# Kernel optimization log

Measured on AMD Instinct MI355X. Metric: run time of the kernel, lower is better.

The kernel has to match this reference:

```python
import jax, jax.numpy as jnp
import numpy as np

ALPHA = 3.0


def _conv3x3(x, W, b):
    # x: [N, C, H, W]; W: [O, I, 3, 3]; SAME padding, stride 1 (matches Conv2d(dim, dim, 3, 1, 1))
    y = jax.lax.conv_general_dilated(
        x, W, window_strides=(1, 1), padding='SAME',
        dimension_numbers=('NCHW', 'OIHW', 'NCHW'))
    return y + b[None, :, None, None]


def setup_inputs() -> dict:
    key = jax.random.key(0)
    k = jax.random.split(key, 5)
    b, m, z, x, y = 2, 5, 64, 128, 256
    fan_in = z * 3 * 3
    bound = 1.0 / np.sqrt(fan_in)
    pts = jax.random.normal(k[0], (b, m, z, x, y), dtype=jnp.float32)
    W1 = jax.random.uniform(k[1], (z, z, 3, 3), jnp.float32, -bound, bound)
    b1 = jax.random.uniform(k[2], (z,), jnp.float32, -bound, bound)
    W2 = jax.random.uniform(k[3], (z, z, 3, 3), jnp.float32, -bound, bound)
    b2 = jax.random.uniform(k[4], (z,), jnp.float32, -bound, bound)
    return {"pts": pts, "W1": W1, "b1": b1, "W2": W2, "b2": b2}


def reference(pts, W1, b1, W2, b2):
    b, m, z, x, y = pts.shape
    flat = pts.reshape(b * m, z, x, y)
    n1 = jnp.tanh(ALPHA * _conv3x3(flat, W1, b1)).reshape(b, m, z, x, y)
    n2 = jnp.tanh(ALPHA * _conv3x3(flat, W2, b2)).reshape(b, m, z, x, y)
    # s[b,m,n,x,y] = sum_l n1[b,m,l,x,y] * n2[b,n,l,x,y]; second einsum is s with m,n swapped
    s = jnp.einsum('bmlxy,bnlxy->bmnxy', n1, n2)
    a = s - jnp.swapaxes(s, 1, 2)
    adj = jax.nn.sigmoid(ALPHA * a)
    adj = adj + jnp.eye(m, dtype=adj.dtype)[None, :, :, None, None]
    adj = adj / jnp.sum(adj, axis=2, keepdims=True)
    return adj
```

## Files before the change

### kernel.cpp

```cpp
#include <hip/hip_runtime.h>
#include <hip/hip_bf16.h>

typedef _Float16 f16x8 __attribute__((ext_vector_type(8)));
typedef float f32x4 __attribute__((ext_vector_type(4)));

constexpr int B_ = 2, M_ = 5, C_ = 64, H_ = 128, W_ = 256;
constexpr int HW_ = H_ * W_;
constexpr int PLANE_ = C_ * HW_;
constexpr int NIMG_ = B_ * M_;
constexpr int PH_ = H_ + 2, PW_ = W_ + 2;

constexpr size_t OFF_XIN = 256;
constexpr size_t SZ_XIN  = (size_t)NIMG_ * PH_ * PW_ * 64 * 2;
constexpr size_t OFF_WL1 = OFF_XIN + SZ_XIN;
constexpr size_t SZ_WL   = (size_t)9 * 64 * 64 * 2;
constexpr size_t OFF_WL2 = OFF_WL1 + SZ_WL;
constexpr size_t OFF_N1  = OFF_WL2 + SZ_WL;
constexpr size_t SZ_N    = (size_t)NIMG_ * HW_ * 64 * 2;
constexpr size_t OFF_N2  = OFF_N1 + SZ_N;

__global__ void sniff_kernel(const unsigned short* __restrict__ pts,
                             int* __restrict__ flag) {
  int lane = threadIdx.x;
  unsigned short v = pts[2 * lane];
  int e = (v >> 7) & 0xFF;
  unsigned long long mask = __ballot(e >= 100 && e <= 140);
  if (lane == 0) flag[0] = (__popcll(mask) >= 48) ? 1 : 0;
}

__global__ void border_zero(_Float16* __restrict__ x) {
  int idx = blockIdx.x * 256 + threadIdx.x;
  if (idx >= NIMG_ * 772) return;
  int img = idx / 772, r = idx - img * 772;
  int ph, pw;
  if (r < 258)      { ph = 0;            pw = r; }
  else if (r < 516) { ph = PH_ - 1;      pw = r - 258; }
  else if (r < 644) { ph = r - 516 + 1;  pw = 0; }
  else              { ph = r - 644 + 1;  pw = PW_ - 1; }
  f16x8 z = {};
  _Float16* p = x + ((size_t)(img * PH_ + ph) * PW_ + pw) * 64;
#pragma unroll
  for (int c8 = 0; c8 < 8; ++c8) *(f16x8*)(p + c8 * 8) = z;
}

__global__ __launch_bounds__(256) void prep_kernel(const void* __restrict__ in,
                                                   _Float16* __restrict__ xin,
                                                   const int* __restrict__ flag) {
  __shared__ float sT[64 * 65];
  const int t = threadIdx.x;
  const int wt = blockIdx.x, h = blockIdx.y, img = blockIdx.z;
  const bool isb = flag[0] != 0;
  const size_t ibase = (size_t)img * PLANE_ + (size_t)h * W_ + wt * 64;
#pragma unroll
  for (int k = 0; k < 16; ++k) {
    int idx = k * 256 + t;
    int ic = idx >> 6, w = idx & 63;
    size_t g = ibase + (size_t)ic * HW_ + w;
    float v = isb ? __bfloat162float(((const __hip_bfloat16*)in)[g])
                  : ((const float*)in)[g];
    sT[ic * 65 + w] = v;
  }
  __syncthreads();
#pragma unroll
  for (int k = 0; k < 2; ++k) {
    int idx = k * 256 + t;
    int w = idx >> 3, c8 = idx & 7;
    f16x8 vv;
#pragma unroll
    for (int j = 0; j < 8; ++j) vv[j] = (_Float16)sT[(c8 * 8 + j) * 65 + w];
    int pw = wt * 64 + w + 1;
    size_t rowbase = ((size_t)(img * PH_ + (h + 1)) * PW_ + pw) * 128;
    int off = (c8 * 16) ^ ((pw & 7) << 4);
    *(f16x8*)((char*)xin + rowbase + off) = vv;
  }
}

__global__ void wprep_kernel(const void* __restrict__ W1, const void* __restrict__ W2,
                             _Float16* __restrict__ wl1, _Float16* __restrict__ wl2,
                             const int* __restrict__ flag) {
  int idx = blockIdx.x * 256 + threadIdx.x;
  const bool isb = flag[0] != 0;
  const void* Wsrc = blockIdx.y ? W2 : W1;
  _Float16* dst = blockIdx.y ? wl2 : wl1;
  int tap = idx >> 12;
  int oc = (idx >> 6) & 63;
  int ic = idx & 63;
  size_t s = (size_t)(oc * 64 + ic) * 9 + tap;
  float v = isb ? __bfloat162float(((const __hip_bfloat16*)Wsrc)[s])
                : ((const float*)Wsrc)[s];
  dst[(tap * 4096 + oc * 64 + ic) ^ ((oc & 7) << 3)] = (_Float16)v;
}

__global__ __launch_bounds__(512, 2)
void conv_fused(const _Float16* __restrict__ xin,
                const _Float16* __restrict__ wl1, const _Float16* __restrict__ wl2,
                const void* __restrict__ bias1, const void* __restrict__ bias2,
                const int* __restrict__ flag,
                _Float16* __restrict__ n1, _Float16* __restrict__ n2) {
  __shared__ _Float16 sIn[10 * 66 * 64];
  __shared__ _Float16 sW[2 * 9 * 32 * 64];

  const int t = threadIdx.x;
  const int och = blockIdx.x & 1;
  const int pid = blockIdx.x >> 1;

  const int l = t & 63, wv = t >> 6;
  const int lr = l & 15, hi = l >> 4;
  const bool isb = flag[0] != 0;

#pragma unroll
  for (int c = 0; c < 2; ++c) {
    const f16x8* src = (const f16x8*)((const char*)(c ? wl2 : wl1) + och * 4096);
    f16x8* dst = (f16x8*)sW + c * 2304;
    for (int i = t; i < 2304; i += 512) {
      int tap = i >> 8, e = i & 255;
      dst[i] = src[tap * 512 + e];
    }
  }

  float bv1[2], bv2[2];
#pragma unroll
  for (int ob = 0; ob < 2; ++ob) {
    int oc = och * 32 + ob * 16 + lr;
    bv1[ob] = isb ? __bfloat162float(((const __hip_bfloat16*)bias1)[oc])
                  : ((const float*)bias1)[oc];
    bv2[ob] = isb ? __bfloat162float(((const __hip_bfloat16*)bias2)[oc])
                  : ((const float*)bias2)[oc];
  }

  int c2a[3][2], c2b[2];
#pragma unroll
  for (int dx = 0; dx < 3; ++dx) {
    int key = (((l & 7) + dx) & 7) << 4;
#pragma unroll
    for (int kw = 0; kw < 2; ++kw) c2a[dx][kw] = (hi * 16 + kw * 64) ^ key;
  }
#pragma unroll
  for (int kw = 0; kw < 2; ++kw) c2b[kw] = (hi * 16 + kw * 64) ^ ((l & 7) << 4);

  f16x8 rg[11];
  auto issue = [&](int tt) {
    int img = tt >> 6, hy = (tt >> 2) & 15, wx = tt & 3;
    const f16x8* base = (const f16x8*)(xin + ((size_t)(img * PH_ + hy * 8) * PW_ + wx * 64) * 64);
#pragma unroll
    for (int u = 0; u < 11; ++u) {
      int i = u * 512 + t;
      if (u < 10 || i < 5280) {
        int r = i / 528, cc = i - r * 528;
        rg[u] = base[(size_t)r * (PW_ * 8) + cc];
      }
    }
  };

  issue(pid);

  const char* sInB = (const char*)sIn;
  const char* sWB = (const char*)sW;

#pragma unroll 1
  for (int j = 0; j < 5; ++j) {
    const int tt = pid + 128 * j;

#pragma unroll
    for (int u = 0; u < 11; ++u) {
      int i = u * 512 + t;
      if (u < 10 || i < 5280) ((f16x8*)sIn)[i] = rg[u];
    }
    __syncthreads();

    if (j < 4) issue(pid + 128 * (j + 1));

    f32x4 acc1[4][2], acc2[4][2];
#pragma unroll
    for (int pa = 0; pa < 4; ++pa)
#pragma unroll
      for (int ob = 0; ob < 2; ++ob) {
        acc1[pa][ob] = (f32x4){0.f, 0.f, 0.f, 0.f};
        acc2[pa][ob] = (f32x4){0.f, 0.f, 0.f, 0.f};
      }

#pragma unroll
    for (int ky = 0; ky < 3; ++ky) {
#pragma unroll
      for (int kx = 0; kx < 3; ++kx) {
        const int tap = ky * 3 + kx;
#pragma unroll
        for (int kw = 0; kw < 2; ++kw) {
          f16x8 a[4], b1[2], b2[2];
#pragma unroll
          for (int pa = 0; pa < 4; ++pa)
            a[pa] = *(const f16x8*)(sInB + ((wv + ky) * 8448 + (pa * 16 + lr + kx) * 128 + c2a[kx][kw]));
#pragma unroll
          for (int ob = 0; ob < 2; ++ob) {
            b1[ob] = *(const f16x8*)(sWB + (tap * 4096 + (ob * 16 + lr) * 128 + c2b[kw]));
            b2[ob] = *(const f16x8*)(sWB + (36864 + tap * 4096 + (ob * 16 + lr) * 128 + c2b[kw]));
          }
#pragma unroll
          for (int pa = 0; pa < 4; ++pa)
#pragma unroll
            for (int ob = 0; ob < 2; ++ob) {
              acc1[pa][ob] = __builtin_amdgcn_mfma_f32_16x16x32_f16(a[pa], b1[ob], acc1[pa][ob], 0, 0, 0);
              acc2[pa][ob] = __builtin_amdgcn_mfma_f32_16x16x32_f16(a[pa], b2[ob], acc2[pa][ob], 0, 0, 0);
            }
        }
      }
    }

    {
      int img = tt >> 6, hy = (tt >> 2) & 15, wx = tt & 3;
      size_t rowbase = ((size_t)(img * H_ + hy * 8 + wv) * W_ + wx * 64) * 64 + och * 32 + lr;
#pragma unroll
      for (int pa = 0; pa < 4; ++pa)
#pragma unroll
        for (int ob = 0; ob < 2; ++ob)
#pragma unroll
          for (int r = 0; r < 4; ++r) {
            int px = pa * 16 + hi * 4 + r;
            size_t o = rowbase + (size_t)px * 64 + ob * 16;
            float u1 = acc1[pa][ob][r] + bv1[ob];
            u1 = fminf(fmaxf(u1, -8.f), 8.f);
            float e1 = __builtin_exp2f(u1 * -8.656170245f);
            n1[o] = (_Float16)((1.f - e1) * __builtin_amdgcn_rcpf(1.f + e1));
            float u2 = acc2[pa][ob][r] + bv2[ob];
            u2 = fminf(fmaxf(u2, -8.f), 8.f);
            float e2 = __builtin_exp2f(u2 * -8.656170245f);
            n2[o] = (_Float16)((1.f - e2) * __builtin_amdgcn_rcpf(1.f + e2));
          }
    }
    __syncthreads();
  }
}

__global__ __launch_bounds__(256)
void pairwise_kernel(const _Float16* __restrict__ n1, const _Float16* __restrict__ n2,
                     void* __restrict__ out, const int* __restrict__ flag) {
  int tid = blockIdx.x * 256 + threadIdx.x;
  int gp = tid >> 3;
  int j = tid & 7;
  int b = gp >> 15, px = gp & (HW_ - 1);
  const _Float16* p1 = n1 + ((size_t)(b * M_) * HW_ + px) * 64 + j * 8;
  const _Float16* p2 = n2 + ((size_t)(b * M_) * HW_ + px) * 64 + j * 8;

  f16x8 A[M_], Bv[M_];
#pragma unroll
  for (int m = 0; m < M_; ++m) {
    A[m]  = *(const f16x8*)(p1 + (size_t)m * PLANE_);
    Bv[m] = *(const f16x8*)(p2 + (size_t)m * PLANE_);
  }

  float s[M_][M_];
#pragma unroll
  for (int m = 0; m < M_; ++m)
#pragma unroll
    for (int n = 0; n < M_; ++n) s[m][n] = 0.f;

#pragma unroll
  for (int jj = 0; jj < 8; ++jj)
#pragma unroll
    for (int m = 0; m < M_; ++m)
#pragma unroll
      for (int n = 0; n < M_; ++n)
        s[m][n] += (float)A[m][jj] * (float)Bv[n][jj];

#pragma unroll
  for (int m = 0; m < M_; ++m)
#pragma unroll
    for (int n = 0; n < M_; ++n) {
      s[m][n] += __shfl_xor(s[m][n], 1);
      s[m][n] += __shfl_xor(s[m][n], 2);
      s[m][n] += __shfl_xor(s[m][n], 4);
    }

  float adj[M_][M_], rs[M_];
#pragma unroll
  for (int m = 0; m < M_; ++m) {
    float r = 0.f;
#pragma unroll
    for (int n = 0; n < M_; ++n) {
      float a = s[m][n] - s[n][m];
      float e = __builtin_exp2f(a * -4.328085123f);
      float v = __builtin_amdgcn_rcpf(1.f + e);
      if (m == n) v += 1.f;
      adj[m][n] = v;
      r += v;
    }
    rs[m] = r;
  }

  const bool isb = flag[0] != 0;
  for (int k = j; k < 25; k += 8) {
    int m = k / 5, n = k - m * 5;
    float v = adj[m][n] * __builtin_amdgcn_rcpf(rs[m]);
    size_t o = ((size_t)((b * M_ + m) * M_ + n)) * HW_ + px;
    if (isb) ((__hip_bfloat16*)out)[o] = __float2bfloat16(v);
    else     ((float*)out)[o] = v;
  }
}

extern "C" void kernel_launch(void* const* d_in, const int* in_sizes, int n_in,
                              void* d_out, int out_size, void* d_ws, size_t ws_size,
                              hipStream_t stream) {
  const void* pts = d_in[0];
  const void* W1  = d_in[1];
  const void* b1  = d_in[2];
  const void* W2  = d_in[3];
  const void* b2  = d_in[4];

  char* ws = (char*)d_ws;
  int* flag = (int*)ws;
  _Float16* xin = (_Float16*)(ws + OFF_XIN);
  _Float16* wl1 = (_Float16*)(ws + OFF_WL1);
  _Float16* wl2 = (_Float16*)(ws + OFF_WL2);
  _Float16* n1  = (_Float16*)(ws + OFF_N1);
  _Float16* n2  = (_Float16*)(ws + OFF_N2);

  sniff_kernel<<<dim3(1), dim3(64), 0, stream>>>((const unsigned short*)pts, flag);
  border_zero<<<dim3((NIMG_ * 772 + 255) / 256), dim3(256), 0, stream>>>(xin);
  prep_kernel<<<dim3(4, H_, NIMG_), dim3(256), 0, stream>>>(pts, xin, flag);
  wprep_kernel<<<dim3(144, 2), dim3(256), 0, stream>>>(W1, W2, wl1, wl2, flag);
  conv_fused<<<dim3(256), dim3(512), 0, stream>>>(xin, wl1, wl2, b1, b2, flag, n1, n2);
  pairwise_kernel<<<dim3(B_ * HW_ * 8 / 256), dim3(256), 0, stream>>>(n1, n2, d_out, flag);
}
```

Baseline: 134.7 us.

## Split conv output channels across twice as many waves per block

Doubles the conv block to 1024 threads, giving each wave one row and one 16-channel half of the output instead of both halves. This halves per-wave accumulators and register staging, which aims to raise occupancy and latency hiding. Bias is folded into the accumulator init, and the tanh epilogue is simplified to one exp and one fma-based reciprocal form without clamping. The trade-off is more waves re-reading the same input fragments from LDS, and the unclamped exp could overflow for large inputs, though the rcp form tolerates infinity.

```diff
diff --git a/kernel.cpp b/kernel.cpp
--- a/kernel.cpp
+++ b/kernel.cpp
@@ -91,7 +91,7 @@
   dst[(tap * 4096 + oc * 64 + ic) ^ ((oc & 7) << 3)] = (_Float16)v;
 }
 
-__global__ __launch_bounds__(512, 2)
+__global__ __launch_bounds__(1024, 4)
 void conv_fused(const _Float16* __restrict__ xin,
                 const _Float16* __restrict__ wl1, const _Float16* __restrict__ wl2,
                 const void* __restrict__ bias1, const void* __restrict__ bias2,
@@ -104,7 +104,10 @@
   const int och = blockIdx.x & 1;
   const int pid = blockIdx.x >> 1;
 
-  const int l = t & 63, wv = t >> 6;
+  const int l = t & 63;
+  const int w = t >> 6;
+  const int row = w >> 1;
+  const int obh = w & 1;
   const int lr = l & 15, hi = l >> 4;
   const bool isb = flag[0] != 0;
 
@@ -112,21 +115,17 @@
   for (int c = 0; c < 2; ++c) {
     const f16x8* src = (const f16x8*)((const char*)(c ? wl2 : wl1) + och * 4096);
     f16x8* dst = (f16x8*)sW + c * 2304;
-    for (int i = t; i < 2304; i += 512) {
+    for (int i = t; i < 2304; i += 1024) {
       int tap = i >> 8, e = i & 255;
       dst[i] = src[tap * 512 + e];
     }
   }
 
-  float bv1[2], bv2[2];
-#pragma unroll
-  for (int ob = 0; ob < 2; ++ob) {
-    int oc = och * 32 + ob * 16 + lr;
-    bv1[ob] = isb ? __bfloat162float(((const __hip_bfloat16*)bias1)[oc])
-                  : ((const float*)bias1)[oc];
-    bv2[ob] = isb ? __bfloat162float(((const __hip_bfloat16*)bias2)[oc])
-                  : ((const float*)bias2)[oc];
-  }
+  const int myoc = och * 32 + obh * 16 + lr;
+  float bv1 = isb ? __bfloat162float(((const __hip_bfloat16*)bias1)[myoc])
+                  : ((const float*)bias1)[myoc];
+  float bv2 = isb ? __bfloat162float(((const __hip_bfloat16*)bias2)[myoc])
+                  : ((const float*)bias2)[myoc];
 
   int c2a[3][2], c2b[2];
 #pragma unroll
@@ -138,14 +137,14 @@
 #pragma unroll
   for (int kw = 0; kw < 2; ++kw) c2b[kw] = (hi * 16 + kw * 64) ^ ((l & 7) << 4);
 
-  f16x8 rg[11];
+  f16x8 rg[6];
   auto issue = [&](int tt) {
     int img = tt >> 6, hy = (tt >> 2) & 15, wx = tt & 3;
     const f16x8* base = (const f16x8*)(xin + ((size_t)(img * PH_ + hy * 8) * PW_ + wx * 64) * 64);
 #pragma unroll
-    for (int u = 0; u < 11; ++u) {
-      int i = u * 512 + t;
-      if (u < 10 || i < 5280) {
+    for (int u = 0; u < 6; ++u) {
+      int i = u * 1024 + t;
+      if (u < 5 || i < 5280) {
         int r = i / 528, cc = i - r * 528;
         rg[u] = base[(size_t)r * (PW_ * 8) + cc];
       }
@@ -156,28 +155,28 @@
 
   const char* sInB = (const char*)sIn;
   const char* sWB = (const char*)sW;
+  const int boff1 = (obh * 16 + lr) * 128;
+  const int boff2 = 36864 + boff1;
 
 #pragma unroll 1
   for (int j = 0; j < 5; ++j) {
     const int tt = pid + 128 * j;
 
 #pragma unroll
-    for (int u = 0; u < 11; ++u) {
-      int i = u * 512 + t;
-      if (u < 10 || i < 5280) ((f16x8*)sIn)[i] = rg[u];
+    for (int u = 0; u < 6; ++u) {
+      int i = u * 1024 + t;
+      if (u < 5 || i < 5280) ((f16x8*)sIn)[i] = rg[u];
     }
     __syncthreads();
 
     if (j < 4) issue(pid + 128 * (j + 1));
 
-    f32x4 acc1[4][2], acc2[4][2];
-#pragma unroll
-    for (int pa = 0; pa < 4; ++pa)
-#pragma unroll
-      for (int ob = 0; ob < 2; ++ob) {
-        acc1[pa][ob] = (f32x4){0.f, 0.f, 0.f, 0.f};
-        acc2[pa][ob] = (f32x4){0.f, 0.f, 0.f, 0.f};
-      }
+    f32x4 acc1[4], acc2[4];
+#pragma unroll
+    for (int pa = 0; pa < 4; ++pa) {
+      acc1[pa] = (f32x4){bv1, bv1, bv1, bv1};
+      acc2[pa] = (f32x4){bv2, bv2, bv2, bv2};
+    }
 
 #pragma unroll
     for (int ky = 0; ky < 3; ++ky) {
@@ -186,46 +185,35 @@
         const int tap = ky * 3 + kx;
 #pragma unroll
         for (int kw = 0; kw < 2; ++kw) {
-          f16x8 a[4], b1[2], b2[2];
+          f16x8 a[4], b1, b2;
 #pragma unroll
           for (int pa = 0; pa < 4; ++pa)
-            a[pa] = *(const f16x8*)(sInB + ((wv + ky) * 8448 + (pa * 16 + lr + kx) * 128 + c2a[kx][kw]));
-#pragma unroll
-          for (int ob = 0; ob < 2; ++ob) {
-            b1[ob] = *(const f16x8*)(sWB + (tap * 4096 + (ob * 16 + lr) * 128 + c2b[kw]));
-            b2[ob] = *(const f16x8*)(sWB + (36864 + tap * 4096 + (ob * 16 + lr) * 128 + c2b[kw]));
+            a[pa] = *(const f16x8*)(sInB + ((row + ky) * 8448 + (pa * 16 + lr + kx) * 128 + c2a[kx][kw]));
+          b1 = *(const f16x8*)(sWB + tap * 4096 + boff1 + c2b[kw]);
+          b2 = *(const f16x8*)(sWB + tap * 4096 + boff2 + c2b[kw]);
+#pragma unroll
+          for (int pa = 0; pa < 4; ++pa) {
+            acc1[pa] = __builtin_amdgcn_mfma_f32_16x16x32_f16(a[pa], b1, acc1[pa], 0, 0, 0);
+            acc2[pa] = __builtin_amdgcn_mfma_f32_16x16x32_f16(a[pa], b2, acc2[pa], 0, 0, 0);
           }
-#pragma unroll
-          for (int pa = 0; pa < 4; ++pa)
-#pragma unroll
-            for (int ob = 0; ob < 2; ++ob) {
-              acc1[pa][ob] = __builtin_amdgcn_mfma_f32_16x16x32_f16(a[pa], b1[ob], acc1[pa][ob], 0, 0, 0);
-              acc2[pa][ob] = __builtin_amdgcn_mfma_f32_16x16x32_f16(a[pa], b2[ob], acc2[pa][ob], 0, 0, 0);
-            }
         }
       }
     }
 
     {
       int img = tt >> 6, hy = (tt >> 2) & 15, wx = tt & 3;
-      size_t rowbase = ((size_t)(img * H_ + hy * 8 + wv) * W_ + wx * 64) * 64 + och * 32 + lr;
+      size_t rowbase = ((size_t)(img * H_ + hy * 8 + row) * W_ + wx * 64) * 64 + myoc;
 #pragma unroll
       for (int pa = 0; pa < 4; ++pa)
 #pragma unroll
-        for (int ob = 0; ob < 2; ++ob)
-#pragma unroll
-          for (int r = 0; r < 4; ++r) {
-            int px = pa * 16 + hi * 4 + r;
-            size_t o = rowbase + (size_t)px * 64 + ob * 16;
-            float u1 = acc1[pa][ob][r] + bv1[ob];
-            u1 = fminf(fmaxf(u1, -8.f), 8.f);
-            float e1 = __builtin_exp2f(u1 * -8.656170245f);
-            n1[o] = (_Float16)((1.f - e1) * __builtin_amdgcn_rcpf(1.f + e1));
-            float u2 = acc2[pa][ob][r] + bv2[ob];
-            u2 = fminf(fmaxf(u2, -8.f), 8.f);
-            float e2 = __builtin_exp2f(u2 * -8.656170245f);
-            n2[o] = (_Float16)((1.f - e2) * __builtin_amdgcn_rcpf(1.f + e2));
-          }
+        for (int r = 0; r < 4; ++r) {
+          int px = pa * 16 + hi * 4 + r;
+          size_t o = rowbase + (size_t)px * 64;
+          float e1 = __builtin_exp2f(acc1[pa][r] * 8.656170245f);
+          n1[o] = (_Float16)fmaf(-2.f, __builtin_amdgcn_rcpf(1.f + e1), 1.f);
+          float e2 = __builtin_exp2f(acc2[pa][r] * 8.656170245f);
+          n2[o] = (_Float16)fmaf(-2.f, __builtin_amdgcn_rcpf(1.f + e2), 1.f);
+        }
     }
     __syncthreads();
   }
@@ -318,6 +306,6 @@
   border_zero<<<dim3((NIMG_ * 772 + 255) / 256), dim3(256), 0, stream>>>(xin);
   prep_kernel<<<dim3(4, H_, NIMG_), dim3(256), 0, stream>>>(pts, xin, flag);
   wprep_kernel<<<dim3(144, 2), dim3(256), 0, stream>>>(W1, W2, wl1, wl2, flag);
-  conv_fused<<<dim3(256), dim3(512), 0, stream>>>(xin, wl1, wl2, b1, b2, flag, n1, n2);
+  conv_fused<<<dim3(256), dim3(1024), 0, stream>>>(xin, wl1, wl2, b1, b2, flag, n1, n2);
   pairwise_kernel<<<dim3(B_ * HW_ * 8 / 256), dim3(256), 0, stream>>>(n1, n2, d_out, flag);
 }
```

Result: slower. 144.6 us (+7.4%).

## Stage conv input via direct global-to-LDS loads and cache W1 fragments in registers

Applied to the files above, without the earlier changes.

Replaces the register-staged prefetch of the next input tile with direct global_load_lds copies issued right before each tile's compute, followed by a full vmcnt wait. This drops the cross-iteration overlap in exchange for fewer VGPRs. Most of the W1 B-fragments are hoisted into registers for the whole kernel, cutting LDS reads. Bias is folded into the accumulator init, and tanh is rewritten as 1-2/(1+exp(2x)) without clamping. The risks are exposed load latency, higher register pressure from the cached fragments, and possible overflow of exp for large inputs, although rcp of inf yields 0 so the result stays bounded.

```diff
diff --git a/kernel.cpp b/kernel.cpp
--- a/kernel.cpp
+++ b/kernel.cpp
@@ -138,45 +138,52 @@
 #pragma unroll
   for (int kw = 0; kw < 2; ++kw) c2b[kw] = (hi * 16 + kw * 64) ^ ((l & 7) << 4);
 
-  f16x8 rg[11];
-  auto issue = [&](int tt) {
-    int img = tt >> 6, hy = (tt >> 2) & 15, wx = tt & 3;
-    const f16x8* base = (const f16x8*)(xin + ((size_t)(img * PH_ + hy * 8) * PW_ + wx * 64) * 64);
-#pragma unroll
-    for (int u = 0; u < 11; ++u) {
-      int i = u * 512 + t;
-      if (u < 10 || i < 5280) {
-        int r = i / 528, cc = i - r * 528;
-        rg[u] = base[(size_t)r * (PW_ * 8) + cc];
-      }
-    }
-  };
-
-  issue(pid);
-
   const char* sInB = (const char*)sIn;
   const char* sWB = (const char*)sW;
+
+  __syncthreads();
+
+  f16x8 b1r0[9][2];
+  f16x8 b1r1[9];
+#pragma unroll
+  for (int tap = 0; tap < 9; ++tap) {
+#pragma unroll
+    for (int kw = 0; kw < 2; ++kw)
+      b1r0[tap][kw] = *(const f16x8*)(sWB + tap * 4096 + lr * 128 + c2b[kw]);
+    b1r1[tap] = *(const f16x8*)(sWB + tap * 4096 + (16 + lr) * 128 + c2b[0]);
+  }
+
+  auto stage = [&](int tt) {
+    int img = tt >> 6, hy = (tt >> 2) & 15, wx = tt & 3;
+    const _Float16* tb = xin + ((size_t)(img * PH_ + hy * 8) * PW_ + wx * 64) * 64;
+#pragma unroll
+    for (int u = 0; u < 11; ++u) {
+      int c = u * 512 + t;
+      if (u < 10 || c < 5280) {
+        int r = c / 528, cc = c - r * 528;
+        const _Float16* g = tb + (size_t)r * (PW_ * 64) + cc * 8;
+        __builtin_amdgcn_global_load_lds(
+            (const __attribute__((address_space(1))) void*)g,
+            (__attribute__((address_space(3))) void*)(sIn + c * 8), 16, 0, 0);
+      }
+    }
+  };
 
 #pragma unroll 1
   for (int j = 0; j < 5; ++j) {
     const int tt = pid + 128 * j;
 
-#pragma unroll
-    for (int u = 0; u < 11; ++u) {
-      int i = u * 512 + t;
-      if (u < 10 || i < 5280) ((f16x8*)sIn)[i] = rg[u];
-    }
+    stage(tt);
+    asm volatile("s_waitcnt vmcnt(0)" ::: "memory");
     __syncthreads();
 
-    if (j < 4) issue(pid + 128 * (j + 1));
-
     f32x4 acc1[4][2], acc2[4][2];
 #pragma unroll
     for (int pa = 0; pa < 4; ++pa)
 #pragma unroll
       for (int ob = 0; ob < 2; ++ob) {
-        acc1[pa][ob] = (f32x4){0.f, 0.f, 0.f, 0.f};
-        acc2[pa][ob] = (f32x4){0.f, 0.f, 0.f, 0.f};
+        acc1[pa][ob] = (f32x4){bv1[ob], bv1[ob], bv1[ob], bv1[ob]};
+        acc2[pa][ob] = (f32x4){bv2[ob], bv2[ob], bv2[ob], bv2[ob]};
       }
 
 #pragma unroll
@@ -186,22 +193,22 @@
         const int tap = ky * 3 + kx;
 #pragma unroll
         for (int kw = 0; kw < 2; ++kw) {
-          f16x8 a[4], b1[2], b2[2];
+          f16x8 a[4];
 #pragma unroll
           for (int pa = 0; pa < 4; ++pa)
             a[pa] = *(const f16x8*)(sInB + ((wv + ky) * 8448 + (pa * 16 + lr + kx) * 128 + c2a[kx][kw]));
-#pragma unroll
-          for (int ob = 0; ob < 2; ++ob) {
-            b1[ob] = *(const f16x8*)(sWB + (tap * 4096 + (ob * 16 + lr) * 128 + c2b[kw]));
-            b2[ob] = *(const f16x8*)(sWB + (36864 + tap * 4096 + (ob * 16 + lr) * 128 + c2b[kw]));
+          f16x8 b1a = b1r0[tap][kw];
+          f16x8 b1b = (kw == 0) ? b1r1[tap]
+                                : *(const f16x8*)(sWB + tap * 4096 + (16 + lr) * 128 + c2b[1]);
+          f16x8 b2a = *(const f16x8*)(sWB + 36864 + tap * 4096 + lr * 128 + c2b[kw]);
+          f16x8 b2b = *(const f16x8*)(sWB + 36864 + tap * 4096 + (16 + lr) * 128 + c2b[kw]);
+#pragma unroll
+          for (int pa = 0; pa < 4; ++pa) {
+            acc1[pa][0] = __builtin_amdgcn_mfma_f32_16x16x32_f16(a[pa], b1a, acc1[pa][0], 0, 0, 0);
+            acc1[pa][1] = __builtin_amdgcn_mfma_f32_16x16x32_f16(a[pa], b1b, acc1[pa][1], 0, 0, 0);
+            acc2[pa][0] = __builtin_amdgcn_mfma_f32_16x16x32_f16(a[pa], b2a, acc2[pa][0], 0, 0, 0);
+            acc2[pa][1] = __builtin_amdgcn_mfma_f32_16x16x32_f16(a[pa], b2b, acc2[pa][1], 0, 0, 0);
           }
-#pragma unroll
-          for (int pa = 0; pa < 4; ++pa)
-#pragma unroll
-            for (int ob = 0; ob < 2; ++ob) {
-              acc1[pa][ob] = __builtin_amdgcn_mfma_f32_16x16x32_f16(a[pa], b1[ob], acc1[pa][ob], 0, 0, 0);
-              acc2[pa][ob] = __builtin_amdgcn_mfma_f32_16x16x32_f16(a[pa], b2[ob], acc2[pa][ob], 0, 0, 0);
-            }
         }
       }
     }
@@ -217,14 +224,10 @@
           for (int r = 0; r < 4; ++r) {
             int px = pa * 16 + hi * 4 + r;
             size_t o = rowbase + (size_t)px * 64 + ob * 16;
-            float u1 = acc1[pa][ob][r] + bv1[ob];
-            u1 = fminf(fmaxf(u1, -8.f), 8.f);
-            float e1 = __builtin_exp2f(u1 * -8.656170245f);
-            n1[o] = (_Float16)((1.f - e1) * __builtin_amdgcn_rcpf(1.f + e1));
-            float u2 = acc2[pa][ob][r] + bv2[ob];
-            u2 = fminf(fmaxf(u2, -8.f), 8.f);
-            float e2 = __builtin_exp2f(u2 * -8.656170245f);
-            n2[o] = (_Float16)((1.f - e2) * __builtin_amdgcn_rcpf(1.f + e2));
+            float e1 = __builtin_exp2f(acc1[pa][ob][r] * 8.656170245f);
+            n1[o] = (_Float16)fmaf(-2.f, __builtin_amdgcn_rcpf(1.f + e1), 1.f);
+            float e2 = __builtin_exp2f(acc2[pa][ob][r] * 8.656170245f);
+            n2[o] = (_Float16)fmaf(-2.f, __builtin_amdgcn_rcpf(1.f + e2), 1.f);
           }
     }
     __syncthreads();
```

Result: slower. 182.5 us (+35.4%).
